# Kernel tuning notes

Measured on AMD Instinct MI355X. Metric: run time of the kernel, lower is better.

Reference implementation:

```python
import jax, jax.numpy as jnp
import numpy as np
from jax import lax

FX, FY = 518.857, 519.469   # NYU-v2 depth intrinsics (cx/cy unused by forward)
B, H, W = 8, 479, 639       # TRAIN_CROP_SIZE = [W, H]; H+1, W+1 divisible by 4
P = 8                       # even PATCH_SIZE -> box-filter output is [H+1, W+1]
EPS = 1e-6


def _coords():
    # u_u0 = x - W/2, v_v0 = y - H/2, broadcast over [B,1,H,W]
    u = jnp.arange(W, dtype=jnp.float32)[None, None, None, :] - W / 2.0
    v = jnp.arange(H, dtype=jnp.float32)[None, None, :, None] - H / 2.0
    return u, v


def _surface_normal(xyz):
    # xyz: [H, W, 3] -> normals [H, W, 3]
    x, y, z = xyz[..., 0], xyz[..., 1], xyz[..., 2]
    # 9 box-filtered moments in a single depthwise conv (the original does 9 conv2d calls)
    mom = jnp.stack([x * x, x * y, x * z, y * y, y * z, z * z, x, y, z], 0)[None]  # [1,9,H,W]
    kern = jnp.ones((9, 1, P, P), xyz.dtype)
    s = lax.conv_general_dilated(mom, kern, (1, 1), [(P // 2, P // 2)] * 2,
                                 feature_group_count=9)[0]  # [9, H+1, W+1]
    xx, xy, xz, yy, yz, zz, xs, ys, zs = s
    ATA = jnp.stack([xx, xy, xz, xy, yy, yz, xz, yz, zz], -1)  # [H+1, W+1, 9]
    Hp, Wp = ATA.shape[0], ATA.shape[1]
    ATA = ATA.reshape(Hp, Wp, 3, 3) + EPS * jnp.eye(3, dtype=xyz.dtype)
    AT1 = jnp.stack([xs, ys, zs], -1)[..., None]  # [H+1, W+1, 3, 1]
    # original loops over 4x4 sub-patches with overlap=0 -> equivalent full-grid solve
    n = jnp.linalg.solve(ATA, AT1)                # [H+1, W+1, 3, 1]
    n = n / jnp.sqrt(jnp.sum(n * n, axis=2, keepdims=True))
    n = n[:-1, :-1, :, 0]                         # [H, W, 3]
    # orient toward camera: flip where dot(n, xyz) > 0
    flip = jnp.sum(n * xyz, axis=2, keepdims=True) > 0
    return jnp.where(flip, -n, n)


def _fit_normals(depth):
    # depth: [B,1,H,W] -> surface normals [B,3,H,W], zeroed where depth <= 0
    u, v = _coords()
    x = u * depth / FX
    y = v * depth / FY
    xyz = jnp.concatenate([x, y, depth], 1).transpose(0, 2, 3, 1)  # [B,H,W,3]
    sn = jax.vmap(_surface_normal)(xyz).transpose(0, 3, 1, 2)      # [B,3,H,W]
    return jnp.where(depth > 0, sn, 0.0)


def setup_inputs() -> dict:
    key = jax.random.key(0)
    k1, k2 = jax.random.split(key)
    prediction = jax.random.uniform(k1, (B, 1, H, W), jnp.float32)
    gt = jax.random.uniform(k2, (B, 1, H, W), jnp.float32)
    return {"prediction": prediction, "gt": gt}


def reference(prediction, gt):
    return jnp.mean(jnp.abs(_fit_normals(prediction) - _fit_normals(gt)))
```

## Files before the change

### kernel.cpp

```cpp
#include <hip/hip_runtime.h>

#define HH 479
#define WW 639
#define BATCH 8
#define NBLK (20 * 30 * 8)


__device__ __forceinline__ void solve_normal(
    float xx, float xy, float xz, float yy, float yz, float zz,
    float xs, float ys, float zs,
    float a_c, float b_c, float d0,
    float* nx, float* ny, float* nz)
{
    const float EPSV = 1e-6f;
    const float inv64 = 1.0f / 64.0f;
    float hx = xs * inv64, hy = ys * inv64, hz = zs * inv64;
    float cxx = fmaf(-hx, xs, xx) + EPSV;
    float cxy = fmaf(-hx, ys, xy);
    float cxz = fmaf(-hx, zs, xz);
    float cyy = fmaf(-hy, ys, yy) + EPSV;
    float cyz = fmaf(-hy, zs, yz);
    float czz = fmaf(-hz, zs, zz) + EPSV;
    float c00 = fmaf(cyy, czz, -cyz * cyz);
    float c01 = fmaf(cxz, cyz, -cxy * czz);
    float c02 = fmaf(cxy, cyz, -cxz * cyy);
    float c11 = fmaf(cxx, czz, -cxz * cxz);
    float c12 = fmaf(cxy, cxz, -cxx * cyz);
    float c22 = fmaf(cxx, cyy, -cxy * cxy);
    float m0 = fmaf(c00, xs, fmaf(c01, ys, c02 * zs));
    float m1 = fmaf(c01, xs, fmaf(c11, ys, c12 * zs));
    float m2 = fmaf(c02, xs, fmaf(c12, ys, c22 * zs));
    float g  = fmaf(m0, a_c, fmaf(m1, b_c, m2));
    float inv = rsqrtf(fmaf(m0, m0, fmaf(m1, m1, m2 * m2)));
    if (g > 0.0f) inv = -inv;
    if (!(d0 > 0.0f)) inv = 0.0f;
    *nx = m0 * inv; *ny = m1 * inv; *nz = m2 * inv;
}

__global__ __launch_bounds__(256, 4)
void ppal_main(const float* __restrict__ pred, const float* __restrict__ gt,
               double* __restrict__ acc)
{
    const int tx = threadIdx.x;
    const int ty = threadIdx.y;
    const int tid = ty * 16 + tx;
    const int j0 = blockIdx.x * 32;
    const int i0 = blockIdx.y * 16;
    const int b  = blockIdx.z;

    const float invFX = 1.0f / 518.857f;
    const float invFY = 1.0f / 519.469f;

    __shared__ float sd[2][23 * 40];
    __shared__ float cs[2][624 * 6];

    const float* src0 = pred + (size_t)b * (HH * WW);
    const float* src1 = gt   + (size_t)b * (HH * WW);
    for (int idx = tid; idx < 23 * 40; idx += 256) {
        int lr = idx / 40, lc = idx - lr * 40;
        int r = i0 - 4 + lr, c = j0 - 4 + lc;
        bool ok = (lc < 39) && (r >= 0) && (r < HH) && (c >= 0) && (c < WW);
        int off = r * WW + c;
        sd[0][idx] = ok ? src0[off] : 0.0f;
        sd[1][idx] = ok ? src1[off] : 0.0f;
    }
    __syncthreads();

    if (tid < 156) {
        int k  = tid >= 78;
        int rm = tid - 78 * k;
        int h  = rm >= 39;
        int c  = rm - 39 * h;
        int rbase = 8 * h;
        float S1 = 0.f, Sb = 0.f, Sbb = 0.f, T1 = 0.f, Tb = 0.f;
#pragma unroll
        for (int r = 0; r < 8; ++r) {
            int rr = rbase + r;
            float d  = sd[k][rr * 40 + c];
            float bv = ((float)(i0 + rr - 4) - 239.5f) * invFY;
            float bd = bv * d;
            T1 += d;  Tb += bd;
            S1  = fmaf(d,  d,  S1);
            Sb  = fmaf(bd, d,  Sb);
            Sbb = fmaf(bd, bd, Sbb);
        }
        {
            float* e = &cs[k][6 * (rbase * 39 + c)];
            *(float2*)(e)     = make_float2(S1, Sb);
            *(float2*)(e + 2) = make_float2(Sbb, T1);
            e[4] = Tb;
        }
#pragma unroll
        for (int s = 1; s < 8; ++s) {
            int i = rbase + s;
            float d0 = sd[k][(i - 1) * 40 + c];
            float d1 = sd[k][(i + 7) * 40 + c];
            float b0 = ((float)(i0 + i - 5)  - 239.5f) * invFY;
            float b1 = ((float)(i0 + i + 3)  - 239.5f) * invFY;
            float bd0 = b0 * d0, bd1 = b1 * d1;
            T1 += d1 - d0;
            Tb += bd1 - bd0;
            S1  += fmaf(d1,  d1,  -d0  * d0);
            Sb  += fmaf(bd1, d1,  -bd0 * d0);
            Sbb += fmaf(bd1, bd1, -bd0 * bd0);
            float* e = &cs[k][6 * (i * 39 + c)];
            *(float2*)(e)     = make_float2(S1, Sb);
            *(float2*)(e + 2) = make_float2(Sbb, T1);
            e[4] = Tb;
        }
    }
    __syncthreads();

    const int i  = i0 + ty;
    const int jl = j0 + 2 * tx;
    const bool valid0 = (i < HH);
    const bool valid1 = (i < HH) && (jl + 1 < WW);

    float aw[9], aw2[9];
#pragma unroll
    for (int m = 0; m < 9; ++m) {
        float a = ((float)(jl + m - 4) - 319.5f) * invFX;
        aw[m] = a;
        aw2[m] = a * a;
    }
    float bc = ((float)i - 239.5f) * invFY;
    const int ebase = ty * 39 + 2 * tx;

    float n0A[3], n1A[3];
    float contrib = 0.0f;
#pragma unroll
    for (int k = 0; k < 2; ++k) {
        float Sxx = 0.f, Sxy = 0.f, Sxz = 0.f, Syy = 0.f, Syz = 0.f, Szz = 0.f;
        float Sxs = 0.f, Sys = 0.f, Szs = 0.f;
#pragma unroll
        for (int m = 1; m < 8; ++m) {
            const float* e = &cs[k][6 * (ebase + m)];
            float2 p01 = *(const float2*)(e);
            float2 p23 = *(const float2*)(e + 2);
            float  tb  = e[4];
            Szz += p01.x;  Syz += p01.y;  Syy += p23.x;
            Szs += p23.y;  Sys += tb;
            Sxz = fmaf(aw[m],  p01.x, Sxz);
            Sxy = fmaf(aw[m],  p01.y, Sxy);
            Sxs = fmaf(aw[m],  p23.y, Sxs);
            Sxx = fmaf(aw2[m], p01.x, Sxx);
        }

        float nn[2][3];
#pragma unroll
        for (int p = 0; p < 2; ++p) {
            int m = (p == 0) ? 0 : 8;
            const float* e = &cs[k][6 * (ebase + m)];
            float2 p01 = *(const float2*)(e);
            float2 p23 = *(const float2*)(e + 2);
            float  tb  = e[4];
            float xx = fmaf(aw2[m], p01.x, Sxx);
            float xy = fmaf(aw[m],  p01.y, Sxy);
            float xz = fmaf(aw[m],  p01.x, Sxz);
            float yy = Syy + p23.x;
            float yz = Syz + p01.y;
            float zz = Szz + p01.x;
            float xs = fmaf(aw[m],  p23.y, Sxs);
            float ys = Sys + tb;
            float zs = Szs + p23.y;
            float d0 = sd[k][(ty + 4) * 40 + (2 * tx + p + 4)];
            solve_normal(xx, xy, xz, yy, yz, zz, xs, ys, zs,
                         aw[4 + p], bc, d0, &nn[p][0], &nn[p][1], &nn[p][2]);
        }
        if (k == 0) {
            n0A[0] = nn[0][0]; n0A[1] = nn[0][1]; n0A[2] = nn[0][2];
            n1A[0] = nn[1][0]; n1A[1] = nn[1][1]; n1A[2] = nn[1][2];
        } else {
            float c0 = fabsf(n0A[0] - nn[0][0]) + fabsf(n0A[1] - nn[0][1])
                     + fabsf(n0A[2] - nn[0][2]);
            float c1 = fabsf(n1A[0] - nn[1][0]) + fabsf(n1A[1] - nn[1][1])
                     + fabsf(n1A[2] - nn[1][2]);
            contrib = (valid0 ? c0 : 0.0f) + (valid1 ? c1 : 0.0f);
        }
    }

    float v = contrib;
#pragma unroll
    for (int off = 32; off > 0; off >>= 1) v += __shfl_down(v, off, 64);
    __shared__ float wsum[4];
    int wid = tid >> 6, lane = tid & 63;
    if (lane == 0) wsum[wid] = v;
    __syncthreads();
    if (tid == 0) {
        double bs = (double)wsum[0] + (double)wsum[1] + (double)wsum[2] + (double)wsum[3];
        int slot = blockIdx.x + 20 * blockIdx.y + 600 * blockIdx.z;
        acc[slot] = bs;
    }
}

__global__ void ppal_finalize(const double* __restrict__ acc, float* __restrict__ out)
{
    int tid = threadIdx.x;
    double v = 0.0;
    for (int s = tid; s < NBLK; s += 256) v += acc[s];
#pragma unroll
    for (int off = 32; off > 0; off >>= 1) v += __shfl_down(v, off, 64);
    __shared__ double wsum[4];
    int wid = tid >> 6, lane = tid & 63;
    if (lane == 0) wsum[wid] = v;
    __syncthreads();
    if (tid == 0)
        out[0] = (float)((wsum[0] + wsum[1] + wsum[2] + wsum[3])
                         * (1.0 / 7345944.0));
}

extern "C" void kernel_launch(void* const* d_in, const int* in_sizes, int n_in,
                              void* d_out, int out_size, void* d_ws, size_t ws_size,
                              hipStream_t stream)
{
    const float* pred = (const float*)d_in[0];
    const float* gt   = (const float*)d_in[1];
    float* out  = (float*)d_out;
    double* acc = (double*)d_ws;

    dim3 grid(20, 30, BATCH);
    dim3 block(16, 16);
    ppal_main<<<grid, block, 0, stream>>>(pred, gt, acc);
    ppal_finalize<<<1, 256, 0, stream>>>(acc, out);
}
```

Measured before the change: 100.6 us.

## Process pred and gt sequentially with a single shared column-sum buffer

The column-sum shared buffer is halved by handling the prediction and ground-truth images one after another, with extra barriers between the phases. The launch-bounds occupancy hint rises from 4 to 6 blocks. Each column thread now covers rows in an interleaved pattern and steps two rows per iteration, and aw² is recomputed inline instead of kept in a separate array. The goal is to cut LDS and register pressure so more blocks fit per CU, at the cost of serialising the two images and adding synchronisation.

```diff
diff --git a/kernel.cpp b/kernel.cpp
--- a/kernel.cpp
+++ b/kernel.cpp
@@ -37,7 +37,7 @@
     *nx = m0 * inv; *ny = m1 * inv; *nz = m2 * inv;
 }
 
-__global__ __launch_bounds__(256, 4)
+__global__ __launch_bounds__(256, 6)
 void ppal_main(const float* __restrict__ pred, const float* __restrict__ gt,
                double* __restrict__ acc)
 {
@@ -52,7 +52,8 @@
     const float invFY = 1.0f / 519.469f;
 
     __shared__ float sd[2][23 * 40];
-    __shared__ float cs[2][624 * 6];
+    __shared__ float cs[624 * 6];
+    __shared__ float wsum[4];
 
     const float* src0 = pred + (size_t)b * (HH * WW);
     const float* src1 = gt   + (size_t)b * (HH * WW);
@@ -64,125 +65,129 @@
         sd[0][idx] = ok ? src0[off] : 0.0f;
         sd[1][idx] = ok ? src1[off] : 0.0f;
     }
+
+    float aw[9];
+#pragma unroll
+    for (int m = 0; m < 9; ++m)
+        aw[m] = ((float)(j0 + 2 * tx + m - 4) - 319.5f) * invFX;
+    const float bc = ((float)(i0 + ty) - 239.5f) * invFY;
+    const int ebase = ty * 39 + 2 * tx;
+
+    float n0A[3], n1A[3];
+    float contrib = 0.0f;
+
     __syncthreads();
 
-    if (tid < 156) {
-        int k  = tid >= 78;
-        int rm = tid - 78 * k;
-        int h  = rm >= 39;
-        int c  = rm - 39 * h;
-        int rbase = 8 * h;
-        float S1 = 0.f, Sb = 0.f, Sbb = 0.f, T1 = 0.f, Tb = 0.f;
-#pragma unroll
-        for (int r = 0; r < 8; ++r) {
-            int rr = rbase + r;
-            float d  = sd[k][rr * 40 + c];
-            float bv = ((float)(i0 + rr - 4) - 239.5f) * invFY;
-            float bd = bv * d;
-            T1 += d;  Tb += bd;
-            S1  = fmaf(d,  d,  S1);
-            Sb  = fmaf(bd, d,  Sb);
-            Sbb = fmaf(bd, bd, Sbb);
+#pragma unroll
+    for (int k = 0; k < 2; ++k) {
+        if (tid < 156) {
+            int g = tid / 39;
+            int c = tid - 39 * g;
+            int rb = 8 * (g >> 1) + (g & 1);
+            const float* col = &sd[k][c];
+            float S1 = 0.f, Sb = 0.f, Sbb = 0.f, T1 = 0.f, Tb = 0.f;
+#pragma unroll
+            for (int r = 0; r < 8; ++r) {
+                int rr = rb + r;
+                float d  = col[rr * 40];
+                float bv = ((float)(i0 + rr - 4) - 239.5f) * invFY;
+                float bd = bv * d;
+                T1 += d;  Tb += bd;
+                S1  = fmaf(d,  d,  S1);
+                Sb  = fmaf(bd, d,  Sb);
+                Sbb = fmaf(bd, bd, Sbb);
+            }
+            {
+                float* e = &cs[6 * (rb * 39 + c)];
+                *(float2*)(e)     = make_float2(S1, Sb);
+                *(float2*)(e + 2) = make_float2(Sbb, T1);
+                e[4] = Tb;
+            }
+#pragma unroll
+            for (int s = 1; s < 4; ++s) {
+                int i = rb + 2 * s;
+                float d0a = col[(i - 2) * 40], d0b = col[(i - 1) * 40];
+                float d1a = col[(i + 6) * 40], d1b = col[(i + 7) * 40];
+                float b0a = ((float)(i0 + i - 6) - 239.5f) * invFY;
+                float b0b = ((float)(i0 + i - 5) - 239.5f) * invFY;
+                float b1a = ((float)(i0 + i + 2) - 239.5f) * invFY;
+                float b1b = ((float)(i0 + i + 3) - 239.5f) * invFY;
+                float bd0a = b0a * d0a, bd0b = b0b * d0b;
+                float bd1a = b1a * d1a, bd1b = b1b * d1b;
+                T1  += (d1a - d0a) + (d1b - d0b);
+                Tb  += (bd1a - bd0a) + (bd1b - bd0b);
+                S1  += fmaf(d1a, d1a, -d0a * d0a)
+                     + fmaf(d1b, d1b, -d0b * d0b);
+                Sb  += fmaf(bd1a, d1a, -bd0a * d0a)
+                     + fmaf(bd1b, d1b, -bd0b * d0b);
+                Sbb += fmaf(bd1a, bd1a, -bd0a * bd0a)
+                     + fmaf(bd1b, bd1b, -bd0b * bd0b);
+                float* e = &cs[6 * (i * 39 + c)];
+                *(float2*)(e)     = make_float2(S1, Sb);
+                *(float2*)(e + 2) = make_float2(Sbb, T1);
+                e[4] = Tb;
+            }
         }
+        __syncthreads();
+
         {
-            float* e = &cs[k][6 * (rbase * 39 + c)];
-            *(float2*)(e)     = make_float2(S1, Sb);
-            *(float2*)(e + 2) = make_float2(Sbb, T1);
-            e[4] = Tb;
-        }
-#pragma unroll
-        for (int s = 1; s < 8; ++s) {
-            int i = rbase + s;
-            float d0 = sd[k][(i - 1) * 40 + c];
-            float d1 = sd[k][(i + 7) * 40 + c];
-            float b0 = ((float)(i0 + i - 5)  - 239.5f) * invFY;
-            float b1 = ((float)(i0 + i + 3)  - 239.5f) * invFY;
-            float bd0 = b0 * d0, bd1 = b1 * d1;
-            T1 += d1 - d0;
-            Tb += bd1 - bd0;
-            S1  += fmaf(d1,  d1,  -d0  * d0);
-            Sb  += fmaf(bd1, d1,  -bd0 * d0);
-            Sbb += fmaf(bd1, bd1, -bd0 * bd0);
-            float* e = &cs[k][6 * (i * 39 + c)];
-            *(float2*)(e)     = make_float2(S1, Sb);
-            *(float2*)(e + 2) = make_float2(Sbb, T1);
-            e[4] = Tb;
+            float Sxx = 0.f, Sxy = 0.f, Sxz = 0.f, Syy = 0.f, Syz = 0.f;
+            float Szz = 0.f, Sxs = 0.f, Sys = 0.f, Szs = 0.f;
+#pragma unroll
+            for (int m = 1; m < 8; ++m) {
+                const float* e = &cs[6 * (ebase + m)];
+                float2 p01 = *(const float2*)(e);
+                float2 p23 = *(const float2*)(e + 2);
+                float  tb  = e[4];
+                Szz += p01.x;  Syz += p01.y;  Syy += p23.x;
+                Szs += p23.y;  Sys += tb;
+                Sxz = fmaf(aw[m],         p01.x, Sxz);
+                Sxy = fmaf(aw[m],         p01.y, Sxy);
+                Sxs = fmaf(aw[m],         p23.y, Sxs);
+                Sxx = fmaf(aw[m] * aw[m], p01.x, Sxx);
+            }
+
+            float nn[2][3];
+#pragma unroll
+            for (int p = 0; p < 2; ++p) {
+                int m = (p == 0) ? 0 : 8;
+                const float* e = &cs[6 * (ebase + m)];
+                float2 p01 = *(const float2*)(e);
+                float2 p23 = *(const float2*)(e + 2);
+                float  tb  = e[4];
+                float xx = fmaf(aw[m] * aw[m], p01.x, Sxx);
+                float xy = fmaf(aw[m], p01.y, Sxy);
+                float xz = fmaf(aw[m], p01.x, Sxz);
+                float yy = Syy + p23.x;
+                float yz = Syz + p01.y;
+                float zz = Szz + p01.x;
+                float xs = fmaf(aw[m], p23.y, Sxs);
+                float ys = Sys + tb;
+                float zs = Szs + p23.y;
+                float d0 = sd[k][(ty + 4) * 40 + (2 * tx + p + 4)];
+                solve_normal(xx, xy, xz, yy, yz, zz, xs, ys, zs,
+                             aw[4 + p], bc, d0, &nn[p][0], &nn[p][1], &nn[p][2]);
+            }
+            if (k == 0) {
+                n0A[0] = nn[0][0]; n0A[1] = nn[0][1]; n0A[2] = nn[0][2];
+                n1A[0] = nn[1][0]; n1A[1] = nn[1][1]; n1A[2] = nn[1][2];
+                __syncthreads();
+            } else {
+                const int i = i0 + ty;
+                const bool valid0 = (i < HH);
+                const bool valid1 = (i < HH) && (j0 + 2 * tx + 1 < WW);
+                float c0 = fabsf(n0A[0] - nn[0][0]) + fabsf(n0A[1] - nn[0][1])
+                         + fabsf(n0A[2] - nn[0][2]);
+                float c1 = fabsf(n1A[0] - nn[1][0]) + fabsf(n1A[1] - nn[1][1])
+                         + fabsf(n1A[2] - nn[1][2]);
+                contrib = (valid0 ? c0 : 0.0f) + (valid1 ? c1 : 0.0f);
+            }
         }
     }
-    __syncthreads();
-
-    const int i  = i0 + ty;
-    const int jl = j0 + 2 * tx;
-    const bool valid0 = (i < HH);
-    const bool valid1 = (i < HH) && (jl + 1 < WW);
-
-    float aw[9], aw2[9];
-#pragma unroll
-    for (int m = 0; m < 9; ++m) {
-        float a = ((float)(jl + m - 4) - 319.5f) * invFX;
-        aw[m] = a;
-        aw2[m] = a * a;
-    }
-    float bc = ((float)i - 239.5f) * invFY;
-    const int ebase = ty * 39 + 2 * tx;
-
-    float n0A[3], n1A[3];
-    float contrib = 0.0f;
-#pragma unroll
-    for (int k = 0; k < 2; ++k) {
-        float Sxx = 0.f, Sxy = 0.f, Sxz = 0.f, Syy = 0.f, Syz = 0.f, Szz = 0.f;
-        float Sxs = 0.f, Sys = 0.f, Szs = 0.f;
-#pragma unroll
-        for (int m = 1; m < 8; ++m) {
-            const float* e = &cs[k][6 * (ebase + m)];
-            float2 p01 = *(const float2*)(e);
-            float2 p23 = *(const float2*)(e + 2);
-            float  tb  = e[4];
-            Szz += p01.x;  Syz += p01.y;  Syy += p23.x;
-            Szs += p23.y;  Sys += tb;
-            Sxz = fmaf(aw[m],  p01.x, Sxz);
-            Sxy = fmaf(aw[m],  p01.y, Sxy);
-            Sxs = fmaf(aw[m],  p23.y, Sxs);
-            Sxx = fmaf(aw2[m], p01.x, Sxx);
-        }
-
-        float nn[2][3];
-#pragma unroll
-        for (int p = 0; p < 2; ++p) {
-            int m = (p == 0) ? 0 : 8;
-            const float* e = &cs[k][6 * (ebase + m)];
-            float2 p01 = *(const float2*)(e);
-            float2 p23 = *(const float2*)(e + 2);
-            float  tb  = e[4];
-            float xx = fmaf(aw2[m], p01.x, Sxx);
-            float xy = fmaf(aw[m],  p01.y, Sxy);
-            float xz = fmaf(aw[m],  p01.x, Sxz);
-            float yy = Syy + p23.x;
-            float yz = Syz + p01.y;
-            float zz = Szz + p01.x;
-            float xs = fmaf(aw[m],  p23.y, Sxs);
-            float ys = Sys + tb;
-            float zs = Szs + p23.y;
-            float d0 = sd[k][(ty + 4) * 40 + (2 * tx + p + 4)];
-            solve_normal(xx, xy, xz, yy, yz, zz, xs, ys, zs,
-                         aw[4 + p], bc, d0, &nn[p][0], &nn[p][1], &nn[p][2]);
-        }
-        if (k == 0) {
-            n0A[0] = nn[0][0]; n0A[1] = nn[0][1]; n0A[2] = nn[0][2];
-            n1A[0] = nn[1][0]; n1A[1] = nn[1][1]; n1A[2] = nn[1][2];
-        } else {
-            float c0 = fabsf(n0A[0] - nn[0][0]) + fabsf(n0A[1] - nn[0][1])
-                     + fabsf(n0A[2] - nn[0][2]);
-            float c1 = fabsf(n1A[0] - nn[1][0]) + fabsf(n1A[1] - nn[1][1])
-                     + fabsf(n1A[2] - nn[1][2]);
-            contrib = (valid0 ? c0 : 0.0f) + (valid1 ? c1 : 0.0f);
-        }
-    }
 
     float v = contrib;
 #pragma unroll
     for (int off = 32; off > 0; off >>= 1) v += __shfl_down(v, off, 64);
-    __shared__ float wsum[4];
     int wid = tid >> 6, lane = tid & 63;
     if (lane == 0) wsum[wid] = v;
     __syncthreads();
```

New measurement: 106.7 us. +6.0%, slower.
